# Performance work log

Hardware: AMD Instinct MI355X
Metric: run time of the kernel (lower is better)

## Reference

```python
import jax, jax.numpy as jnp
import numpy as np

DIM = 1024
HEADS = 16
HEAD_DIM = DIM // HEADS
SCALE = HEAD_DIM ** -0.5


def setup_inputs() -> dict:
    key = jax.random.key(0)
    ks = jax.random.split(key, 9)
    b, n, m = 4, 1024, 1024
    x = jax.random.normal(ks[0], (b, n, DIM), dtype=jnp.float32)
    context = jax.random.normal(ks[1], (b, m, DIM), dtype=jnp.float32)
    mask = jax.random.randint(ks[2], (b, n, 32, 32), 0, 2, dtype=jnp.int32)
    s = DIM ** -0.5
    Wq = jax.random.normal(ks[3], (DIM, DIM), dtype=jnp.float32) * s
    bq = jnp.zeros((DIM,), dtype=jnp.float32)
    Wkv = jax.random.normal(ks[4], (DIM, 2 * DIM), dtype=jnp.float32) * s
    bkv = jnp.zeros((2 * DIM,), dtype=jnp.float32)
    Wp = jax.random.normal(ks[5], (DIM, DIM), dtype=jnp.float32) * s
    bp = jnp.zeros((DIM,), dtype=jnp.float32)
    return {"x": x, "context": context, "mask": mask,
            "Wq": Wq, "bq": bq, "Wkv": Wkv, "bkv": bkv, "Wp": Wp, "bp": bp}


def reference(x, context, mask, Wq, bq, Wkv, bkv, Wp, bp):
    b, n, _ = x.shape
    m = context.shape[1]
    h, d = HEADS, HEAD_DIM
    # projections
    q = (x @ Wq + bq).reshape(b, n, h, d).transpose(0, 2, 1, 3)       # [b,h,n,d]
    kv = (context @ Wkv + bkv).reshape(b, m, 2, h, d)
    k = kv[:, :, 0].transpose(0, 2, 1, 3)                              # [b,h,m,d]
    v = kv[:, :, 1].transpose(0, 2, 1, 3)                              # [b,h,m,d]
    dots = jnp.einsum('bhnd,bhmd->bhnm', q, k) * SCALE                 # [b,h,n,m]
    # mask: [b,n,H,W] -> [b,1,n,m]; masked_fill where mask == 0
    mflat = mask.reshape(b, n, m)[:, None]                             # [b,1,n,m]
    dots = jnp.where(mflat == 0, -jnp.inf, dots)
    attn = jax.nn.softmax(dots, axis=-1)
    out = jnp.einsum('bhnm,bhmd->bhnd', attn, v)
    out = out.transpose(0, 2, 1, 3).reshape(b, n, h * d)
    return out @ Wp + bp
```

## Files before the change

### kernel.cpp

```cpp
#include <hip/hip_runtime.h>

typedef __bf16 bf16;
typedef __bf16 bf16x8 __attribute__((ext_vector_type(8)));
typedef float f32x4 __attribute__((ext_vector_type(4)));
typedef unsigned long long u64;

#define MFMA16(a, b, c) __builtin_amdgcn_mfma_f32_16x16x32_bf16(a, b, c, 0, 0, 0)

__device__ __forceinline__ void gl_lds16(const void* g, void* l) {
  __builtin_amdgcn_global_load_lds(
      (const __attribute__((address_space(1))) unsigned int*)g,
      (__attribute__((address_space(3))) unsigned int*)l, 16, 0, 0);
}

__global__ __launch_bounds__(256)
void prep_k(const float* __restrict__ Wq, const float* __restrict__ Wkv,
            const float* __restrict__ Wp, const int* __restrict__ mask,
            bf16* __restrict__ BqkvT, bf16* __restrict__ WpT,
            u64* __restrict__ maskbits) {
  const int bx = blockIdx.x;
  const int tid = threadIdx.x;
  if (bx >= 1024) {
    const int idx = (bx - 1024) * 256 + tid;
    const int4* p = (const int4*)(mask + (size_t)idx * 64);
    u64 v = 0;
#pragma unroll
    for (int i = 0; i < 16; ++i) {
      int4 m = p[i];
      v |= (u64)(m.x != 0) << (4 * i);
      v |= (u64)(m.y != 0) << (4 * i + 1);
      v |= (u64)(m.z != 0) << (4 * i + 2);
      v |= (u64)(m.w != 0) << (4 * i + 3);
    }
    maskbits[idx] = v;
    return;
  }
  const int ct = bx >> 4, rt = bx & 15;
  const float* src;
  bf16* dst;
  int C, c0, drow0;
  if (ct < 16) {
    src = Wq; C = 1024; c0 = ct * 64; dst = BqkvT; drow0 = c0;
  } else if (ct < 48) {
    src = Wkv; C = 2048; c0 = (ct - 16) * 64; dst = BqkvT; drow0 = 1024 + c0;
  } else {
    src = Wp; C = 1024; c0 = (ct - 48) * 64; dst = WpT; drow0 = c0;
  }
  __shared__ bf16 T[64][72];
  const int r0 = rt * 64;
#pragma unroll
  for (int i = 0; i < 2; ++i) {
    int c = i * 256 + tid;
    int row = c >> 3, col = (c & 7) * 8;
    const float* sp = &src[(size_t)(r0 + row) * C + c0 + col];
    f32x4 a0 = *(const f32x4*)sp;
    f32x4 a1 = *(const f32x4*)(sp + 4);
    bf16x8 t;
#pragma unroll
    for (int j = 0; j < 4; ++j) { t[j] = (bf16)a0[j]; t[4 + j] = (bf16)a1[j]; }
    *(bf16x8*)&T[row][col] = t;
  }
  __syncthreads();
#pragma unroll
  for (int i = 0; i < 2; ++i) {
    int c = i * 256 + tid;
    int orow = c >> 3, ocol = (c & 7) * 8;
    bf16x8 v;
#pragma unroll
    for (int j = 0; j < 8; ++j) v[j] = T[ocol + j][orow];
    *(bf16x8*)&dst[(size_t)(drow0 + orow) * 1024 + r0 + ocol] = v;
  }
}

template <int EPI>
__global__ __launch_bounds__(256)
void gemm_sw(const float* __restrict__ Af0, const float* __restrict__ Af1,
             const bf16* __restrict__ Ab, const bf16* __restrict__ Bt,
             const float* __restrict__ bias0, const float* __restrict__ bias1,
             bf16* __restrict__ oq, bf16* __restrict__ ok,
             bf16* __restrict__ ovt, float* __restrict__ outf) {
  __shared__ bf16 As[64][64];
  __shared__ bf16 Bs[128][64];
  const int tid = threadIdx.x;
  const int lane = tid & 63;
  const int w = tid >> 6;
  const int wm = (w >> 1) * 32, wn = (w & 1) * 64;
  const int l15 = lane & 15, l4 = lane >> 4;
  const int lrow = lane >> 3;
  const int scol = ((lane & 7) ^ (lrow & 7)) * 8;
  const int m0 = blockIdx.x * 64;
  const int n0 = blockIdx.y * 128;

  const float* Asrc = (EPI == 1) ? ((n0 < 1024) ? Af0 : Af1) : nullptr;

  const int ar = tid >> 2;
  const int acb = (tid & 3) * 2;

  f32x4 acc[2][4] = {};

  for (int kk = 0; kk < 1024; kk += 64) {
#pragma unroll
    for (int it = 0; it < 4; ++it) {
      const int r = w * 32 + it * 8;
      gl_lds16(&Bt[(size_t)(n0 + r + lrow) * 1024 + kk + scol], &Bs[r][0]);
    }
    if (EPI == 0) {
#pragma unroll
      for (int it = 0; it < 2; ++it) {
        const int r = w * 16 + it * 8;
        gl_lds16(&Ab[(size_t)(m0 + r + lrow) * 1024 + kk + scol], &As[r][0]);
      }
    } else {
#pragma unroll
      for (int j = 0; j < 2; ++j) {
        const int cbL = acb + j;
        const float* ap = &Asrc[(size_t)(m0 + ar) * 1024 + kk + cbL * 8];
        f32x4 a0 = *(const f32x4*)ap;
        f32x4 a1 = *(const f32x4*)(ap + 4);
        bf16x8 t;
#pragma unroll
        for (int u = 0; u < 4; ++u) { t[u] = (bf16)a0[u]; t[4 + u] = (bf16)a1[u]; }
        *(bf16x8*)&As[ar][(cbL ^ (ar & 7)) * 8] = t;
      }
    }
    __syncthreads();
#pragma unroll
    for (int ks = 0; ks < 2; ++ks) {
      const int sw = ((ks * 4 + l4) ^ (l15 & 7)) * 8;
      bf16x8 af[2], bfr[4];
#pragma unroll
      for (int i = 0; i < 2; ++i)
        af[i] = *(const bf16x8*)&As[wm + i * 16 + l15][sw];
#pragma unroll
      for (int j = 0; j < 4; ++j)
        bfr[j] = *(const bf16x8*)&Bs[wn + j * 16 + l15][sw];
#pragma unroll
      for (int i = 0; i < 2; ++i)
#pragma unroll
        for (int j = 0; j < 4; ++j)
          acc[i][j] = MFMA16(af[i], bfr[j], acc[i][j]);
    }
    __syncthreads();
  }

  const float SCALE2 = 0.18033688011112042f;
#pragma unroll
  for (int j = 0; j < 4; ++j) {
    const int col = n0 + wn + j * 16 + l15;
    float bc;
    if (EPI == 1) bc = (col < 1024) ? bias0[col] : bias1[col - 1024];
    else bc = bias0[col];
#pragma unroll
    for (int i = 0; i < 2; ++i) {
#pragma unroll
      for (int r = 0; r < 4; ++r) {
        const int row = m0 + wm + i * 16 + l4 * 4 + r;
        const float v = acc[i][j][r] + bc;
        if (EPI == 0) {
          outf[(size_t)row * 1024 + col] = v;
        } else {
          const int b = row >> 10, n = row & 1023;
          if (col < 1024) {
            const int h = col >> 6, d = col & 63;
            oq[(((size_t)(b * 16 + h)) * 1024 + n) * 64 + d] =
                (bf16)(v * SCALE2);
          } else {
            const int ckv = col - 1024;
            const int s = ckv >> 10, c2 = ckv & 1023;
            const int h = c2 >> 6, d = c2 & 63;
            if (s == 0)
              ok[(((size_t)(b * 16 + h)) * 1024 + n) * 64 + d] = (bf16)v;
            else
              ovt[(((size_t)(b * 16 + h)) * 64 + d) * 1024 + n] = (bf16)v;
          }
        }
      }
    }
  }
}

__global__ __launch_bounds__(256)
void attn_kernel(const bf16* __restrict__ q, const bf16* __restrict__ k,
                 const bf16* __restrict__ vT, const u64* __restrict__ maskbits,
                 bf16* __restrict__ ao) {
  const int bh = blockIdx.x;
  const int ntile = blockIdx.y;
  const int b = bh >> 4, h = bh & 15;
  const int tid = threadIdx.x;
  const int lane = tid & 63;
  const int w = tid >> 6;
  const int l15 = lane & 15, l4 = lane >> 4;

  __shared__ bf16 Ks[64][72];
  __shared__ bf16 Vts[64][72];
  __shared__ bf16 Pw[4][16][72];

  const size_t base = (size_t)bh * 65536;
  const int nrow0 = ntile * 64 + w * 16;

  bf16x8 qf[2];
#pragma unroll
  for (int ks = 0; ks < 2; ++ks)
    qf[ks] =
        *(const bf16x8*)&q[base + (size_t)(nrow0 + l15) * 64 + ks * 32 + l4 * 8];

  f32x4 o[4] = {};
  float lsum[4] = {0.0f, 0.0f, 0.0f, 0.0f};

  const u64* mb = maskbits + (size_t)(b * 1024 + nrow0) * 16;

  for (int mt = 0; mt < 16; ++mt) {
#pragma unroll
    for (int i = 0; i < 2; ++i) {
      int c = i * 256 + tid;
      int row = c >> 3, col = (c & 7) * 8;
      *(bf16x8*)&Ks[row][col] =
          *(const bf16x8*)&k[base + (size_t)(mt * 64 + row) * 64 + col];
      *(bf16x8*)&Vts[row][col] =
          *(const bf16x8*)&vT[base + (size_t)row * 1024 + mt * 64 + col];
    }
    __syncthreads();

    f32x4 s[4];
#pragma unroll
    for (int sub = 0; sub < 4; ++sub) s[sub] = f32x4{-12.f, -12.f, -12.f, -12.f};
#pragma unroll
    for (int ks = 0; ks < 2; ++ks) {
#pragma unroll
      for (int sub = 0; sub < 4; ++sub) {
        bf16x8 bfr = *(const bf16x8*)&Ks[sub * 16 + l15][ks * 32 + l4 * 8];
        s[sub] = MFMA16(qf[ks], bfr, s[sub]);
      }
    }

    u64 wbits[4];
#pragma unroll
    for (int r = 0; r < 4; ++r) wbits[r] = mb[(size_t)(l4 * 4 + r) * 16 + mt];

#pragma unroll
    for (int sub = 0; sub < 4; ++sub) {
#pragma unroll
      for (int r = 0; r < 4; ++r) {
        float p = exp2f(s[sub][r]);
        p = ((wbits[r] >> (sub * 16 + l15)) & 1) ? p : 0.0f;
        lsum[r] += p;
        Pw[w][l4 * 4 + r][sub * 16 + l15] = (bf16)p;
      }
    }

#pragma unroll
    for (int ks = 0; ks < 2; ++ks) {
      bf16x8 af = *(const bf16x8*)&Pw[w][l15][ks * 32 + l4 * 8];
#pragma unroll
      for (int sub = 0; sub < 4; ++sub) {
        bf16x8 bfr = *(const bf16x8*)&Vts[sub * 16 + l15][ks * 32 + l4 * 8];
        o[sub] = MFMA16(af, bfr, o[sub]);
      }
    }
    __syncthreads();
  }

  float inv[4];
#pragma unroll
  for (int r = 0; r < 4; ++r) {
    float t = lsum[r];
#pragma unroll
    for (int d = 1; d < 16; d <<= 1) t += __shfl_xor(t, d);
    inv[r] = 1.0f / t;
  }

#pragma unroll
  for (int sub = 0; sub < 4; ++sub) {
#pragma unroll
    for (int r = 0; r < 4; ++r) {
      const int n = nrow0 + l4 * 4 + r;
      const size_t idx =
          ((size_t)(b * 1024 + n)) * 1024 + h * 64 + sub * 16 + l15;
      ao[idx] = (bf16)(o[sub][r] * inv[r]);
    }
  }
}

extern "C" void kernel_launch(void* const* d_in, const int* in_sizes, int n_in,
                              void* d_out, int out_size, void* d_ws,
                              size_t ws_size, hipStream_t stream) {
  const float* x = (const float*)d_in[0];
  const float* context = (const float*)d_in[1];
  const int* mask = (const int*)d_in[2];
  const float* Wq = (const float*)d_in[3];
  const float* bq = (const float*)d_in[4];
  const float* Wkv = (const float*)d_in[5];
  const float* bkv = (const float*)d_in[6];
  const float* Wp = (const float*)d_in[7];
  const float* bp = (const float*)d_in[8];
  float* out = (float*)d_out;

  char* ws = (char*)d_ws;
  bf16* BqkvT = (bf16*)(ws);
  bf16* aow = (bf16*)(ws);
  bf16* qw = (bf16*)(ws + (8ull << 20));
  bf16* kw = (bf16*)(ws + (16ull << 20));
  bf16* vtw = (bf16*)(ws + (24ull << 20));
  u64* maskbits = (u64*)(ws + (32ull << 20));
  bf16* WpT = (bf16*)(ws + (33ull << 20));

  const dim3 blk(256);

  prep_k<<<dim3(1280), blk, 0, stream>>>(Wq, Wkv, Wp, mask, BqkvT, WpT,
                                         maskbits);

  gemm_sw<1><<<dim3(64, 24), blk, 0, stream>>>(x, context, nullptr, BqkvT, bq,
                                               bkv, qw, kw, vtw, nullptr);

  attn_kernel<<<dim3(64, 16), blk, 0, stream>>>(qw, kw, vtw, maskbits, aow);

  gemm_sw<0><<<dim3(64, 8), blk, 0, stream>>>(nullptr, nullptr, aow, WpT, bp,
                                              nullptr, nullptr, nullptr,
                                              nullptr, out);
}
```

Measured before the change: 232.1 us.

## Double-buffer GEMM LDS tiles and pre-convert context to bf16 for async loads

Both projection GEMMs now use two LDS buffers so the next K tile is fetched while MFMAs run on the current one, with a single barrier per iteration. The fp32 x operand is prefetched into registers and converted after compute. The context operand is converted to bf16 once in the prep kernel, so the KV part of the QKV GEMM can use direct global-to-LDS loads. This hides load latency and avoids repeated per-tile conversion of context. The cost is doubled shared memory, which may lower occupancy, plus an extra conversion pass in prep.

```diff
diff --git a/kernel.cpp b/kernel.cpp
--- a/kernel.cpp
+++ b/kernel.cpp
@@ -16,10 +16,21 @@
 __global__ __launch_bounds__(256)
 void prep_k(const float* __restrict__ Wq, const float* __restrict__ Wkv,
             const float* __restrict__ Wp, const int* __restrict__ mask,
-            bf16* __restrict__ BqkvT, bf16* __restrict__ WpT,
-            u64* __restrict__ maskbits) {
+            const float* __restrict__ context, bf16* __restrict__ BqkvT,
+            bf16* __restrict__ WpT, u64* __restrict__ maskbits,
+            bf16* __restrict__ cb) {
   const int bx = blockIdx.x;
   const int tid = threadIdx.x;
+  if (bx >= 1280) {
+    const size_t i = ((size_t)(bx - 1280) * 256 + tid) * 8;
+    f32x4 a0 = *(const f32x4*)(context + i);
+    f32x4 a1 = *(const f32x4*)(context + i + 4);
+    bf16x8 t;
+#pragma unroll
+    for (int j = 0; j < 4; ++j) { t[j] = (bf16)a0[j]; t[4 + j] = (bf16)a1[j]; }
+    *(bf16x8*)(cb + i) = t;
+    return;
+  }
   if (bx >= 1024) {
     const int idx = (bx - 1024) * 256 + tid;
     const int4* p = (const int4*)(mask + (size_t)idx * 64);
@@ -74,13 +85,13 @@
 
 template <int EPI>
 __global__ __launch_bounds__(256)
-void gemm_sw(const float* __restrict__ Af0, const float* __restrict__ Af1,
+void gemm_db(const float* __restrict__ Af0, const float* __restrict__ Af1,
              const bf16* __restrict__ Ab, const bf16* __restrict__ Bt,
              const float* __restrict__ bias0, const float* __restrict__ bias1,
              bf16* __restrict__ oq, bf16* __restrict__ ok,
              bf16* __restrict__ ovt, float* __restrict__ outf) {
-  __shared__ bf16 As[64][64];
-  __shared__ bf16 Bs[128][64];
+  __shared__ bf16 As[2][64][64];
+  __shared__ bf16 Bs[2][128][64];
   const int tid = threadIdx.x;
   const int lane = tid & 63;
   const int w = tid >> 6;
@@ -91,56 +102,79 @@
   const int m0 = blockIdx.x * 64;
   const int n0 = blockIdx.y * 128;
 
-  const float* Asrc = (EPI == 1) ? ((n0 < 1024) ? Af0 : Af1) : nullptr;
+  const bool a_async = (EPI == 0) || (n0 >= 1024);
+  const float* Af = (EPI == 1) ? ((n0 < 1024) ? Af0 : Af1) : nullptr;
+  const bf16* Asrc = (EPI == 0) ? Ab : ((const bf16*)Af1);
 
   const int ar = tid >> 2;
   const int acb = (tid & 3) * 2;
 
+  f32x4 pf[4];
   f32x4 acc[2][4] = {};
 
-  for (int kk = 0; kk < 1024; kk += 64) {
-#pragma unroll
-    for (int it = 0; it < 4; ++it) {
-      const int r = w * 32 + it * 8;
-      gl_lds16(&Bt[(size_t)(n0 + r + lrow) * 1024 + kk + scol], &Bs[r][0]);
-    }
-    if (EPI == 0) {
-#pragma unroll
-      for (int it = 0; it < 2; ++it) {
-        const int r = w * 16 + it * 8;
-        gl_lds16(&Ab[(size_t)(m0 + r + lrow) * 1024 + kk + scol], &As[r][0]);
-      }
-    } else {
-#pragma unroll
-      for (int j = 0; j < 2; ++j) {
-        const int cbL = acb + j;
-        const float* ap = &Asrc[(size_t)(m0 + ar) * 1024 + kk + cbL * 8];
-        f32x4 a0 = *(const f32x4*)ap;
-        f32x4 a1 = *(const f32x4*)(ap + 4);
-        bf16x8 t;
-#pragma unroll
-        for (int u = 0; u < 4; ++u) { t[u] = (bf16)a0[u]; t[4 + u] = (bf16)a1[u]; }
-        *(bf16x8*)&As[ar][(cbL ^ (ar & 7)) * 8] = t;
-      }
-    }
+#define STAGE_B(kk, buf)                                                      \
+  _Pragma("unroll") for (int it = 0; it < 4; ++it) {                          \
+    const int r = w * 32 + it * 8;                                            \
+    gl_lds16(&Bt[(size_t)(n0 + r + lrow) * 1024 + (kk) + scol],               \
+             &Bs[buf][r][0]);                                                 \
+  }
+#define STAGE_A_ASYNC(kk, buf)                                                \
+  _Pragma("unroll") for (int it = 0; it < 2; ++it) {                          \
+    const int r = w * 16 + it * 8;                                            \
+    gl_lds16(&Asrc[(size_t)(m0 + r + lrow) * 1024 + (kk) + scol],             \
+             &As[buf][r][0]);                                                 \
+  }
+#define LOAD_A_F32(kk)                                                        \
+  {                                                                           \
+    const float* ap = &Af[(size_t)(m0 + ar) * 1024 + (kk) + acb * 8];         \
+    pf[0] = *(const f32x4*)ap;                                                \
+    pf[1] = *(const f32x4*)(ap + 4);                                          \
+    pf[2] = *(const f32x4*)(ap + 8);                                          \
+    pf[3] = *(const f32x4*)(ap + 12);                                         \
+  }
+#define COMMIT_A_F32(buf)                                                     \
+  _Pragma("unroll") for (int j = 0; j < 2; ++j) {                             \
+    bf16x8 t;                                                                 \
+    _Pragma("unroll") for (int u = 0; u < 4; ++u) {                           \
+      t[u] = (bf16)pf[2 * j][u];                                              \
+      t[4 + u] = (bf16)pf[2 * j + 1][u];                                      \
+    }                                                                         \
+    *(bf16x8*)&As[buf][ar][((acb + j) ^ (ar & 7)) * 8] = t;                   \
+  }
+
+  STAGE_B(0, 0);
+  if (a_async) {
+    STAGE_A_ASYNC(0, 0);
+  } else {
+    LOAD_A_F32(0);
+    COMMIT_A_F32(0);
+  }
+
+  for (int k = 0; k < 16; ++k) {
+    const int cur = k & 1, nxt = cur ^ 1;
+    if (!a_async && k < 15) LOAD_A_F32((k + 1) * 64);
     __syncthreads();
+    if (k < 15) {
+      STAGE_B((k + 1) * 64, nxt);
+      if (a_async) STAGE_A_ASYNC((k + 1) * 64, nxt);
+    }
 #pragma unroll
     for (int ks = 0; ks < 2; ++ks) {
       const int sw = ((ks * 4 + l4) ^ (l15 & 7)) * 8;
       bf16x8 af[2], bfr[4];
 #pragma unroll
       for (int i = 0; i < 2; ++i)
-        af[i] = *(const bf16x8*)&As[wm + i * 16 + l15][sw];
+        af[i] = *(const bf16x8*)&As[cur][wm + i * 16 + l15][sw];
 #pragma unroll
       for (int j = 0; j < 4; ++j)
-        bfr[j] = *(const bf16x8*)&Bs[wn + j * 16 + l15][sw];
+        bfr[j] = *(const bf16x8*)&Bs[cur][wn + j * 16 + l15][sw];
 #pragma unroll
       for (int i = 0; i < 2; ++i)
 #pragma unroll
         for (int j = 0; j < 4; ++j)
           acc[i][j] = MFMA16(af[i], bfr[j], acc[i][j]);
     }
-    __syncthreads();
+    if (!a_async && k < 15) COMMIT_A_F32(nxt);
   }
 
   const float SCALE2 = 0.18033688011112042f;
@@ -177,6 +211,10 @@
       }
     }
   }
+#undef STAGE_B
+#undef STAGE_A_ASYNC
+#undef LOAD_A_F32
+#undef COMMIT_A_F32
 }
 
 __global__ __launch_bounds__(256)
@@ -296,25 +334,27 @@
   float* out = (float*)d_out;
 
   char* ws = (char*)d_ws;
-  bf16* BqkvT = (bf16*)(ws);
+  bf16* cb = (bf16*)(ws);
   bf16* aow = (bf16*)(ws);
-  bf16* qw = (bf16*)(ws + (8ull << 20));
-  bf16* kw = (bf16*)(ws + (16ull << 20));
-  bf16* vtw = (bf16*)(ws + (24ull << 20));
-  u64* maskbits = (u64*)(ws + (32ull << 20));
-  bf16* WpT = (bf16*)(ws + (33ull << 20));
+  bf16* BqkvT = (bf16*)(ws + (8ull << 20));
+  bf16* qw = (bf16*)(ws + (14ull << 20));
+  bf16* kw = (bf16*)(ws + (22ull << 20));
+  bf16* vtw = (bf16*)(ws + (30ull << 20));
+  u64* maskbits = (u64*)(ws + (38ull << 20));
+  bf16* WpT = (bf16*)(ws + (38ull << 20) + (512ull << 10));
 
   const dim3 blk(256);
 
-  prep_k<<<dim3(1280), blk, 0, stream>>>(Wq, Wkv, Wp, mask, BqkvT, WpT,
-                                         maskbits);
-
-  gemm_sw<1><<<dim3(64, 24), blk, 0, stream>>>(x, context, nullptr, BqkvT, bq,
-                                               bkv, qw, kw, vtw, nullptr);
+  prep_k<<<dim3(3328), blk, 0, stream>>>(Wq, Wkv, Wp, mask, context, BqkvT,
+                                         WpT, maskbits, cb);
+
+  gemm_db<1><<<dim3(64, 24), blk, 0, stream>>>(x, (const float*)cb, nullptr,
+                                               BqkvT, bq, bkv, qw, kw, vtw,
+                                               nullptr);
 
   attn_kernel<<<dim3(64, 16), blk, 0, stream>>>(qw, kw, vtw, maskbits, aow);
 
-  gemm_sw<0><<<dim3(64, 8), blk, 0, stream>>>(nullptr, nullptr, aow, WpT, bp,
+  gemm_db<0><<<dim3(64, 8), blk, 0, stream>>>(nullptr, nullptr, aow, WpT, bp,
                                               nullptr, nullptr, nullptr,
                                               nullptr, out);
 }
```

New measurement: 230.7 us. No clear change (-0.6%).
